# Optimization experiments

Hardware: AMD Instinct MI355X
Metric: run time of the kernel (lower is better)

Reference implementation:

```python
import jax, jax.numpy as jnp
import numpy as np

B, L, D = 4, 2048, 768
H, K = 12, 9
IPG = D // H  # in-channels per group = head_size = 64
PAD = (K - 1) // 2


def setup_inputs() -> dict:
    key = jax.random.key(0)
    ks = jax.random.split(key, 8)
    s = lambda k, shape, scale: jax.random.normal(k, shape, dtype=jnp.float32) * scale
    return {
        "query": s(ks[0], (B, L, D), 1.0),
        "dw_w": s(ks[1], (D, 1, K), 0.1),          # depthwise Conv1d weight, no bias
        "pw_w": s(ks[2], (H, IPG, IPG), 0.05),     # grouped 1x1 conv [head, out_pg, in_pg]
        "pw_b": s(ks[3], (D,), 0.02),
        "ak_w": s(ks[4], (H, K, IPG), 0.05),       # conv_attn_kernel grouped 1x1 [head, K, in_pg]
        "ak_b": s(ks[5], (H * K,), 0.02),
        "pt_w": s(ks[6], (D, D), 0.02),            # conv_attn_point Linear weight [out, in]
        "pt_b": s(ks[7], (D,), 0.02),
    }


def _sdconv(query, dw_w, pw_w, pw_b, ak_w, ak_b, pt_w, pt_b):
    b, l, d = query.shape
    # SeparableConv1d: depthwise conv (groups=D, kernel K, padding PAD, no bias)
    x = query.transpose(0, 2, 1)  # [B, D, L]
    dw = jax.lax.conv_general_dilated(
        x, dw_w, window_strides=(1,), padding=[(PAD, PAD)],
        feature_group_count=d, dimension_numbers=("NCH", "OIH", "NCH"))  # [B, D, L]
    # grouped pointwise conv (groups=H, kernel 1)
    dwg = dw.reshape(b, H, IPG, l)
    pw = jnp.einsum("bhil,hoi->bhol", dwg, pw_w).reshape(b, d, l) + pw_b[None, :, None]
    key_conv_attn = pw.transpose(0, 2, 1)  # [B, L, D]
    # stride == 1 path: elementwise gate with query
    conv_attn = key_conv_attn * query  # [B, L, D]
    # conv_attn_kernel: grouped 1x1 conv D -> H*K (per head: IPG -> K)
    ca = conv_attn.reshape(b, l, H, IPG)
    kern = jnp.einsum("blhi,hki->blhk", ca, ak_w) + ak_b.reshape(H, K)  # [B, L, H, K]
    w = jax.nn.softmax(kern, axis=-1)  # softmax over kernel positions
    # conv_attn_point linear on value (= query here)
    v = query @ pt_w.T + pt_b  # [B, L, D]
    # unfold: local windows of size K around each position
    vp = jnp.pad(v, ((0, 0), (PAD, PAD), (0, 0)))
    idx = jnp.arange(l)[:, None] + jnp.arange(K)[None, :]  # [L, K]
    win = vp[:, idx]  # [B, L, K, D]
    winh = win.reshape(b, l, K, H, IPG)
    out = jnp.einsum("blkhd,blhk->blhd", winh, w).reshape(b, l, d)
    return out


def reference(query, dw_w, pw_w, pw_b, ak_w, ak_b, pt_w, pt_b):
    return _sdconv(query, dw_w, pw_w, pw_b, ak_w, ak_b, pt_w, pt_b)
```

## Files before the change

kernel.cpp:

```cpp
#include <hip/hip_runtime.h>
#include <math.h>

#define NB 4
#define NL 2048
#define ND 768
#define NH 12
#define NK 9
#define NIPG 64
#define NPAD 4
#define MT 240

typedef __attribute__((ext_vector_type(8))) short s16x8;
typedef __attribute__((ext_vector_type(4))) float f32x4;

__device__ __forceinline__ unsigned short f2bf(float f) {
  unsigned int u = __float_as_uint(f);
  unsigned int r = (u + 0x7FFFu + ((u >> 16) & 1u)) >> 16;
  return (unsigned short)r;
}
__device__ __forceinline__ float bf2f(unsigned short s) {
  return __uint_as_float(((unsigned int)s) << 16);
}
__device__ __forceinline__ void gload16(const void* g, void* l) {
  __builtin_amdgcn_global_load_lds((const __attribute__((address_space(1))) void*)g,
                                   (__attribute__((address_space(3))) void*)l,
                                   16, 0, 0);
}

__global__ __launch_bounds__(256) void prep(const float* __restrict__ pt_w,
                                            const float* __restrict__ pw_w,
                                            const float* __restrict__ ak_w,
                                            unsigned short* __restrict__ ptb,
                                            unsigned short* __restrict__ pwb,
                                            unsigned short* __restrict__ akp) {
  const int t = blockIdx.x * 256 + threadIdx.x;
  if (t < ND * ND / 4) {
    float4 f = ((const float4*)pt_w)[t];
    ushort4 o; o.x = f2bf(f.x); o.y = f2bf(f.y); o.z = f2bf(f.z); o.w = f2bf(f.w);
    ((ushort4*)ptb)[t] = o;
  }
  if (t < NH * NIPG * NIPG / 4) {
    float4 f = ((const float4*)pw_w)[t];
    ushort4 o; o.x = f2bf(f.x); o.y = f2bf(f.y); o.z = f2bf(f.z); o.w = f2bf(f.w);
    ((ushort4*)pwb)[t] = o;
  }
  if (t < NH * 16 * NIPG) {
    const int h = t >> 10;
    const int r = t & 1023;
    const int k = r >> 6;
    const int i = r & 63;
    akp[t] = (k < NK) ? f2bf(ak_w[((size_t)h * NK + k) * NIPG + i]) : (unsigned short)0;
  }
}

__global__ __launch_bounds__(256) void attn_w(const float* __restrict__ q,
                                              const float* __restrict__ dw_w,
                                              const unsigned short* __restrict__ pwb,
                                              const float* __restrict__ pw_b,
                                              const unsigned short* __restrict__ akp,
                                              const float* __restrict__ ak_b,
                                              float* __restrict__ wout,
                                              unsigned short* __restrict__ qb) {
  __shared__ unsigned short qs[72][68];
  __shared__ unsigned char ab[8192];
  const int l0 = blockIdx.x * 64;
  const int h  = blockIdx.y;
  const int b  = blockIdx.z;
  const int d0 = h * NIPG;
  const int t  = threadIdx.x;
  const int lane = t & 63;
  const int wv = t >> 6;
  const int fr = lane & 15;
  const int fq = lane >> 4;

  const unsigned short* pwh = pwb + (size_t)h * NIPG * NIPG;
  const unsigned short* akh = akp + (size_t)h * 16 * NIPG;
  s16x8 pv0[4], pv1[4];
#pragma unroll
  for (int n = 0; n < 4; ++n) {
    const int o = n * 16 + fr;
    pv0[n] = *(const s16x8*)&pwh[o * 64 + fq * 8];
    pv1[n] = *(const s16x8*)&pwh[o * 64 + 32 + fq * 8];
  }
  s16x8 ak0 = *(const s16x8*)&akh[fr * 64 + fq * 8];
  s16x8 ak1 = *(const s16x8*)&akh[fr * 64 + 32 + fq * 8];
  float dwk[NK];
#pragma unroll
  for (int k = 0; k < NK; ++k) dwk[k] = dw_w[(size_t)(d0 + lane) * NK + k];

  {
    const int sl = t >> 4;
    const int sc = (t & 15) * 4;
    for (int r = sl; r < 72; r += 16) {
      const int l = l0 - NPAD + r;
      ushort4 ub = make_ushort4(0, 0, 0, 0);
      if (l >= 0 && l < NL) {
        float4 val = *(const float4*)&q[((size_t)(b * NL + l)) * ND + d0 + sc];
        ub.x = f2bf(val.x); ub.y = f2bf(val.y); ub.z = f2bf(val.z); ub.w = f2bf(val.w);
        if (r >= NPAD && r < NPAD + 64)
          *(ushort4*)&qb[((size_t)(b * NL + l)) * ND + d0 + sc] = ub;
      }
      *(ushort4*)&qs[r][sc] = ub;
    }
  }
  __syncthreads();

  const int lset = wv * 16;
  {
    float win9[NK];
#pragma unroll
    for (int k = 0; k < NK; ++k) win9[k] = bf2f(qs[lset + k][lane]);
#pragma unroll
    for (int l2 = 0; l2 < 16; ++l2) {
      const int l = lset + l2;
      float s = 0.f;
#pragma unroll
      for (int k = 0; k < NK; ++k) s = fmaf(win9[k], dwk[k], s);
      const int byte = ((l * 64 + lane) * 2) ^ ((l & 7) << 4);
      *(unsigned short*)&ab[byte] = f2bf(s);
      if (l2 < 15) {
#pragma unroll
        for (int k = 0; k < NK - 1; ++k) win9[k] = win9[k + 1];
        win9[NK - 1] = bf2f(qs[lset + l2 + NK][lane]);
      }
    }
  }

  s16x8 av0, av1;
  {
    const int row = lset + fr;
    const int b0 = ((row * 64 + fq * 8) * 2)      ^ ((row & 7) << 4);
    const int b1 = ((row * 64 + 32 + fq * 8) * 2) ^ ((row & 7) << 4);
    av0 = *(const s16x8*)&ab[b0];
    av1 = *(const s16x8*)&ab[b1];
  }
  f32x4 accp[4];
#pragma unroll
  for (int n = 0; n < 4; ++n) {
    accp[n] = (f32x4){0.f, 0.f, 0.f, 0.f};
    accp[n] = __builtin_amdgcn_mfma_f32_16x16x32_bf16(av0, pv0[n], accp[n], 0, 0, 0);
    accp[n] = __builtin_amdgcn_mfma_f32_16x16x32_bf16(av1, pv1[n], accp[n], 0, 0, 0);
  }

#pragma unroll
  for (int n = 0; n < 4; ++n) {
    const int o = n * 16 + fr;
    const float pb = pw_b[d0 + o];
#pragma unroll
    for (int j = 0; j < 4; ++j) {
      const int row = lset + fq * 4 + j;
      const float ca = (accp[n][j] + pb) * bf2f(qs[row + NPAD][o]);
      const int byte = ((row * 64 + o) * 2) ^ ((row & 7) << 4);
      *(unsigned short*)&ab[byte] = f2bf(ca);
    }
  }

  f32x4 acck = (f32x4){0.f, 0.f, 0.f, 0.f};
  {
    const int row = lset + fr;
    const int b0 = ((row * 64 + fq * 8) * 2)      ^ ((row & 7) << 4);
    const int b1 = ((row * 64 + 32 + fq * 8) * 2) ^ ((row & 7) << 4);
    s16x8 a0 = *(const s16x8*)&ab[b0];
    s16x8 a1 = *(const s16x8*)&ab[b1];
    acck = __builtin_amdgcn_mfma_f32_16x16x32_bf16(a0, ak0, acck, 0, 0, 0);
    acck = __builtin_amdgcn_mfma_f32_16x16x32_bf16(a1, ak1, acck, 0, 0, 0);
  }

  const bool kvalid = fr < NK;
  const float akbv = kvalid ? ak_b[h * NK + fr] : 0.f;
#pragma unroll
  for (int j = 0; j < 4; ++j) {
    float val = acck[j] + akbv;
    float mv = kvalid ? val : -3.4e38f;
#pragma unroll
    for (int mm = 1; mm < 16; mm <<= 1) mv = fmaxf(mv, __shfl_xor(mv, mm));
    const float e = kvalid ? __expf(val - mv) : 0.f;
    float ssum = e;
#pragma unroll
    for (int mm = 1; mm < 16; mm <<= 1) ssum += __shfl_xor(ssum, mm);
    if (kvalid) {
      const int row = l0 + lset + fq * 4 + j;
      wout[(((size_t)(b * NL + row)) * NH + h) * NK + fr] = e / ssum;
    }
  }
}

__global__ __launch_bounds__(256, 2) void gemm_conv(const unsigned short* __restrict__ qb,
                                                    const unsigned short* __restrict__ ptb,
                                                    const float* __restrict__ bias,
                                                    const float* __restrict__ w,
                                                    float* __restrict__ out) {
  __shared__ unsigned char smem[75776];
  unsigned short* vt = (unsigned short*)(smem + 40960);
  const int t = threadIdx.x;
  const long mo = (long)blockIdx.x * MT;
  const int n0 = blockIdx.y * 64;
  const int lane = t & 63;
  const int wv = t >> 6;
  const int fr = lane & 15;
  const int fq = lane >> 4;

  const int slotp = (((lane & 3) ^ ((lane >> 3) & 3))) * 16;
  const unsigned char* gA = (const unsigned char*)qb + (mo - 8 + (lane >> 2)) * 1536L + slotp;
  const unsigned char* gB = (const unsigned char*)ptb + (size_t)(n0 + (lane >> 2)) * 1536 + slotp;

  const int srd = (fq ^ ((fr >> 1) & 3)) * 16;
  int aoffb[4], boffb[4];
#pragma unroll
  for (int m = 0; m < 4; ++m) aoffb[m] = (wv * 4 + m) * 1024 + fr * 64 + srd;
#pragma unroll
  for (int n = 0; n < 4; ++n) boffb[n] = 16384 + n * 1024 + fr * 64 + srd;

#define STAGE(kt_)                                                          \
  do {                                                                      \
    unsigned char* sb_ = smem + ((kt_) & 1) * 20480;                        \
    const long kb_ = (long)(kt_) * 64;                                      \
    _Pragma("unroll")                                                       \
    for (int j_ = 0; j_ < 5; ++j_) {                                        \
      const int c_ = wv * 5 + j_;                                           \
      const unsigned char* g_ = (c_ < 16)                                   \
          ? (gA + (long)c_ * 24576 + kb_)                                   \
          : (gB + (long)(c_ - 16) * 24576 + kb_);                           \
      gload16(g_, sb_ + c_ * 1024 + lane * 16);                             \
    }                                                                       \
  } while (0)

#define LOADFRAGS(kt_)                                                      \
  do {                                                                      \
    const unsigned char* sb_ = smem + ((kt_) & 1) * 20480;                  \
    _Pragma("unroll")                                                       \
    for (int m_ = 0; m_ < 4; ++m_) av[m_] = *(const s16x8*)(sb_ + aoffb[m_]); \
    _Pragma("unroll")                                                       \
    for (int n_ = 0; n_ < 4; ++n_) bv[n_] = *(const s16x8*)(sb_ + boffb[n_]); \
  } while (0)

#define MM16                                                                \
  do {                                                                      \
    _Pragma("unroll")                                                       \
    for (int m_ = 0; m_ < 4; ++m_)                                          \
      _Pragma("unroll")                                                     \
      for (int n_ = 0; n_ < 4; ++n_)                                        \
        acc[m_][n_] = __builtin_amdgcn_mfma_f32_16x16x32_bf16(              \
            av[m_], bv[n_], acc[m_][n_], 0, 0, 0);                          \
  } while (0)

  f32x4 acc[4][4] = {};
  s16x8 av[4], bv[4];

  STAGE(0);
  STAGE(1);
  for (int kt = 0; kt < 22; ++kt) {
    asm volatile("s_waitcnt vmcnt(5)" ::: "memory");
    __builtin_amdgcn_s_barrier();
    LOADFRAGS(kt);
    asm volatile("s_waitcnt lgkmcnt(0)" ::: "memory");
    __builtin_amdgcn_sched_barrier(0);
    __builtin_amdgcn_s_barrier();
    STAGE(kt + 2);
    MM16;
  }
  {
    asm volatile("s_waitcnt vmcnt(5)" ::: "memory");
    __builtin_amdgcn_s_barrier();
    LOADFRAGS(22);
    MM16;
  }
  {
    asm volatile("s_waitcnt vmcnt(0)" ::: "memory");
    __builtin_amdgcn_s_barrier();
    LOADFRAGS(23);
    MM16;
  }
#undef STAGE
#undef LOADFRAGS
#undef MM16

#pragma unroll
  for (int m = 0; m < 4; ++m) {
#pragma unroll
    for (int n = 0; n < 4; ++n) {
      const int rb = wv * 64 + m * 16 + fq * 4;
      const int cc = n * 16 + fr;
      const float bbv = bias[n0 + cc];
#pragma unroll
      for (int j = 0; j < 4; ++j)
        vt[(rb + j) * 68 + cc] = f2bf(acc[m][n][j] + bbv);
    }
  }
  __syncthreads();

  const int cq = (t & 15) * 4;
  const int r0 = 8 + (t >> 4) * 15;
  const int h = n0 >> 6;
  float4 win[NK];
#pragma unroll
  for (int k = 0; k < NK; ++k) {
    ushort4 u = *(const ushort4*)&vt[(r0 - 4 + k) * 68 + cq];
    win[k] = make_float4(bf2f(u.x), bf2f(u.y), bf2f(u.z), bf2f(u.w));
  }
#pragma unroll
  for (int i = 0; i < 15; ++i) {
    const int r = r0 + i;
    const long g = mo + r - 8;
    if (g < (long)NB * NL) {
      const int l = (int)(g & (NL - 1));
      const float* wp = &w[((size_t)g * NH + h) * NK];
      float4 a = make_float4(0.f, 0.f, 0.f, 0.f);
#pragma unroll
      for (int k = 0; k < NK; ++k) {
        const int lk = l + k - NPAD;
        if (lk >= 0 && lk < NL) {
          const float wk = wp[k];
          a.x = fmaf(wk, win[k].x, a.x);
          a.y = fmaf(wk, win[k].y, a.y);
          a.z = fmaf(wk, win[k].z, a.z);
          a.w = fmaf(wk, win[k].w, a.w);
        }
      }
      *(float4*)&out[(size_t)g * ND + n0 + cq] = a;
    }
    if (i < 14) {
#pragma unroll
      for (int k = 0; k < NK - 1; ++k) win[k] = win[k + 1];
      ushort4 u = *(const ushort4*)&vt[(r + 5) * 68 + cq];
      win[NK - 1] = make_float4(bf2f(u.x), bf2f(u.y), bf2f(u.z), bf2f(u.w));
    }
  }
}

extern "C" void kernel_launch(void* const* d_in, const int* in_sizes, int n_in,
                              void* d_out, int out_size, void* d_ws, size_t ws_size,
                              hipStream_t stream) {
  const float* query = (const float*)d_in[0];
  const float* dw_w  = (const float*)d_in[1];
  const float* pw_w  = (const float*)d_in[2];
  const float* pw_b  = (const float*)d_in[3];
  const float* ak_w  = (const float*)d_in[4];
  const float* ak_b  = (const float*)d_in[5];
  const float* pt_w  = (const float*)d_in[6];
  const float* pt_b  = (const float*)d_in[7];
  float* out = (float*)d_out;

  float* w = (float*)d_ws;
  unsigned short* qb  = (unsigned short*)(w + (size_t)NB * NL * NH * NK);
  unsigned short* ptb = qb + (size_t)NB * NL * ND;
  unsigned short* pwb = ptb + (size_t)ND * ND;
  unsigned short* akp = pwb + (size_t)NH * NIPG * NIPG;

  prep<<<ND * ND / 4 / 256, 256, 0, stream>>>(pt_w, pw_w, ak_w, ptb, pwb, akp);

  dim3 g2(NL / 64, NH, NB);
  attn_w<<<g2, 256, 0, stream>>>(query, dw_w, pwb, pw_b, akp, ak_b, w, qb);

  dim3 g3((NB * NL + MT - 1) / MT, ND / 64, 1);
  gemm_conv<<<g3, 256, 0, stream>>>(qb, ptb, pt_b, w, out);
}
```

Measured before the change: 160.4 us.

## Stage full B panel in LDS, stream A fragments directly from global with XCD remap

The GEMM now loads the whole 64-column slice of the bf16 pt_w (768x64) into LDS once per block, and reads A (query) fragments straight from global memory into registers in four double-buffered chunks. This replaces the double-buffered LDS pipeline and its per-step barriers. Blocks use a 1D grid with an XCD-aware remap so that neighbouring tiles land on the same XCD for L2 reuse. LDS use rises to about 133KB and the register footprint grows (48 A fragments held live), so occupancy drops to one block per CU. Uncoalesced direct A loads may also cost bandwidth.

```diff
diff --git a/kernel.cpp b/kernel.cpp
--- a/kernel.cpp
+++ b/kernel.cpp
@@ -185,95 +185,78 @@
   }
 }
 
-__global__ __launch_bounds__(256, 2) void gemm_conv(const unsigned short* __restrict__ qb,
-                                                    const unsigned short* __restrict__ ptb,
-                                                    const float* __restrict__ bias,
-                                                    const float* __restrict__ w,
-                                                    float* __restrict__ out) {
-  __shared__ unsigned char smem[75776];
-  unsigned short* vt = (unsigned short*)(smem + 40960);
+__global__ __launch_bounds__(256) void gemm_conv(const unsigned short* __restrict__ qb,
+                                                 const unsigned short* __restrict__ ptb,
+                                                 const float* __restrict__ bias,
+                                                 const float* __restrict__ w,
+                                                 float* __restrict__ out) {
+  __shared__ unsigned char Bl[98304];
+  __shared__ unsigned short vt[256 * 68];
   const int t = threadIdx.x;
-  const long mo = (long)blockIdx.x * MT;
-  const int n0 = blockIdx.y * 64;
+  const int orig = blockIdx.x;
+  const int q8 = 420 >> 3, r8 = 420 & 7;
+  const int xcd = orig & 7, loc = orig >> 3;
+  const int wgid = (xcd < r8 ? xcd * (q8 + 1) : r8 * (q8 + 1) + (xcd - r8) * q8) + loc;
+  const long mo = (long)(wgid / 12) * MT;
+  const int n0 = (wgid % 12) * 64;
   const int lane = t & 63;
   const int wv = t >> 6;
   const int fr = lane & 15;
   const int fq = lane >> 4;
 
-  const int slotp = (((lane & 3) ^ ((lane >> 3) & 3))) * 16;
-  const unsigned char* gA = (const unsigned char*)qb + (mo - 8 + (lane >> 2)) * 1536L + slotp;
-  const unsigned char* gB = (const unsigned char*)ptb + (size_t)(n0 + (lane >> 2)) * 1536 + slotp;
-
-  const int srd = (fq ^ ((fr >> 1) & 3)) * 16;
-  int aoffb[4], boffb[4];
-#pragma unroll
-  for (int m = 0; m < 4; ++m) aoffb[m] = (wv * 4 + m) * 1024 + fr * 64 + srd;
-#pragma unroll
-  for (int n = 0; n < 4; ++n) boffb[n] = 16384 + n * 1024 + fr * 64 + srd;
-
-#define STAGE(kt_)                                                          \
-  do {                                                                      \
-    unsigned char* sb_ = smem + ((kt_) & 1) * 20480;                        \
-    const long kb_ = (long)(kt_) * 64;                                      \
-    _Pragma("unroll")                                                       \
-    for (int j_ = 0; j_ < 5; ++j_) {                                        \
-      const int c_ = wv * 5 + j_;                                           \
-      const unsigned char* g_ = (c_ < 16)                                   \
-          ? (gA + (long)c_ * 24576 + kb_)                                   \
-          : (gB + (long)(c_ - 16) * 24576 + kb_);                           \
-      gload16(g_, sb_ + c_ * 1024 + lane * 16);                             \
-    }                                                                       \
-  } while (0)
-
-#define LOADFRAGS(kt_)                                                      \
-  do {                                                                      \
-    const unsigned char* sb_ = smem + ((kt_) & 1) * 20480;                  \
-    _Pragma("unroll")                                                       \
-    for (int m_ = 0; m_ < 4; ++m_) av[m_] = *(const s16x8*)(sb_ + aoffb[m_]); \
-    _Pragma("unroll")                                                       \
-    for (int n_ = 0; n_ < 4; ++n_) bv[n_] = *(const s16x8*)(sb_ + boffb[n_]); \
-  } while (0)
-
-#define MM16                                                                \
+  {
+    const unsigned char* gsrc =
+        (const unsigned char*)ptb + (size_t)(n0 + (t >> 2)) * 1536 + (t & 3) * 16;
+    unsigned char* ldst = &Bl[t * 16];
+#pragma unroll
+    for (int r = 0; r < 24; ++r)
+      gload16(gsrc + r * 64, ldst + r * 4096);
+  }
+  __builtin_amdgcn_sched_barrier(0);
+
+  const unsigned short* pa = qb + (mo - 8 + wv * 64 + fr) * (long)ND + fq * 8;
+  s16x8 af0[4][6], af1[4][6];
+  f32x4 acc[4][4] = {};
+
+#define LOADA(buf, qq)                                                      \
   do {                                                                      \
     _Pragma("unroll")                                                       \
     for (int m_ = 0; m_ < 4; ++m_)                                          \
       _Pragma("unroll")                                                     \
-      for (int n_ = 0; n_ < 4; ++n_)                                        \
-        acc[m_][n_] = __builtin_amdgcn_mfma_f32_16x16x32_bf16(              \
-            av[m_], bv[n_], acc[m_][n_], 0, 0, 0);                          \
+      for (int j_ = 0; j_ < 6; ++j_)                                        \
+        buf[m_][j_] = *(const s16x8*)(pa + (long)m_ * 16 * ND + ((qq) * 6 + j_) * 32); \
   } while (0)
 
-  f32x4 acc[4][4] = {};
-  s16x8 av[4], bv[4];
-
-  STAGE(0);
-  STAGE(1);
-  for (int kt = 0; kt < 22; ++kt) {
-    asm volatile("s_waitcnt vmcnt(5)" ::: "memory");
-    __builtin_amdgcn_s_barrier();
-    LOADFRAGS(kt);
-    asm volatile("s_waitcnt lgkmcnt(0)" ::: "memory");
-    __builtin_amdgcn_sched_barrier(0);
-    __builtin_amdgcn_s_barrier();
-    STAGE(kt + 2);
-    MM16;
-  }
-  {
-    asm volatile("s_waitcnt vmcnt(5)" ::: "memory");
-    __builtin_amdgcn_s_barrier();
-    LOADFRAGS(22);
-    MM16;
-  }
-  {
-    asm volatile("s_waitcnt vmcnt(0)" ::: "memory");
-    __builtin_amdgcn_s_barrier();
-    LOADFRAGS(23);
-    MM16;
-  }
-#undef STAGE
-#undef LOADFRAGS
-#undef MM16
+#define COMPQ(buf, qq)                                                      \
+  do {                                                                      \
+    _Pragma("unroll")                                                       \
+    for (int j_ = 0; j_ < 6; ++j_) {                                        \
+      const int kt_ = (qq) * 6 + j_;                                        \
+      _Pragma("unroll")                                                     \
+      for (int n_ = 0; n_ < 4; ++n_) {                                      \
+        s16x8 bv_ = *(const s16x8*)&Bl[kt_ * 4096 + (n_ * 16 + fr) * 64 + fq * 16]; \
+        _Pragma("unroll")                                                   \
+        for (int m_ = 0; m_ < 4; ++m_)                                      \
+          acc[m_][n_] = __builtin_amdgcn_mfma_f32_16x16x32_bf16(            \
+              buf[m_][j_], bv_, acc[m_][n_], 0, 0, 0);                      \
+      }                                                                     \
+    }                                                                       \
+  } while (0)
+
+  LOADA(af0, 0);
+  LOADA(af1, 1);
+  asm volatile("s_waitcnt vmcnt(48)" ::: "memory");
+  __builtin_amdgcn_s_barrier();
+  __builtin_amdgcn_sched_barrier(0);
+
+  COMPQ(af0, 0);
+  LOADA(af0, 2);
+  COMPQ(af1, 1);
+  LOADA(af1, 3);
+  COMPQ(af0, 2);
+  COMPQ(af1, 3);
+#undef LOADA
+#undef COMPQ
 
 #pragma unroll
   for (int m = 0; m < 4; ++m) {
@@ -352,6 +335,5 @@
   dim3 g2(NL / 64, NH, NB);
   attn_w<<<g2, 256, 0, stream>>>(query, dw_w, pwb, pw_b, akp, ak_b, w, qb);
 
-  dim3 g3((NB * NL + MT - 1) / MT, ND / 64, 1);
-  gemm_conv<<<g3, 256, 0, stream>>>(qb, ptb, pt_b, w, out);
-}
+  gemm_conv<<<35 * 12, 256, 0, stream>>>(qb, ptb, pt_b, w, out);
+}
```

New measurement: 170.8 us. 6.5% more time.
